# Kernel optimization log

Hardware: AMD Instinct MI355X
Metric: run time of the kernel (lower is better)

The kernel has to match this reference:

```python
import jax, jax.numpy as jnp
import numpy as np

K = 3          # number of nearest neighbors (init kwarg k)
EPS = 1e-16    # PyG knn_interpolate clamps squared distance at 1e-16


def setup_inputs() -> dict:
    key = jax.random.key(0)
    ks = jax.random.split(key, 8)
    N, M, C_IN, C_SKIP, H = 4096, 16384, 256, 128, 256
    x = jax.random.normal(ks[0], (N, C_IN), dtype=jnp.float32)
    pos = jax.random.normal(ks[1], (N, 3), dtype=jnp.float32)
    x_skip = jax.random.normal(ks[2], (M, C_SKIP), dtype=jnp.float32)
    pos_skip = jax.random.normal(ks[3], (M, 3), dtype=jnp.float32)
    W1 = jax.random.normal(ks[4], (C_IN + C_SKIP, H), dtype=jnp.float32) * (1.0 / np.sqrt(C_IN + C_SKIP))
    b1 = jnp.zeros((H,), dtype=jnp.float32)
    W2 = jax.random.normal(ks[5], (H, H), dtype=jnp.float32) * (1.0 / np.sqrt(H))
    b2 = jnp.zeros((H,), dtype=jnp.float32)
    return {"x": x, "pos": pos, "x_skip": x_skip, "pos_skip": pos_skip,
            "W1": W1, "b1": b1, "W2": W2, "b2": b2}


def knn_interpolate(x, pos, pos_skip):
    # squared pairwise distances [M, N]
    d2 = (jnp.sum(pos_skip * pos_skip, -1, keepdims=True)
          - 2.0 * pos_skip @ pos.T
          + jnp.sum(pos * pos, -1))
    neg_d, idx = jax.lax.top_k(-d2, K)          # k smallest distances
    w = 1.0 / jnp.maximum(-neg_d, EPS)           # [M, K] inverse-distance weights
    feats = x[idx]                               # [M, K, C] gather
    return jnp.einsum('mk,mkc->mc', w, feats) / jnp.sum(w, -1, keepdims=True)


def reference(x, pos, x_skip, pos_skip, W1, b1, W2, b2):
    y = knn_interpolate(x, pos, pos_skip)                # [M, C_in]
    h = jnp.concatenate([y, x_skip], axis=-1)            # [M, C_in + C_skip]
    h = jax.nn.relu(h @ W1 + b1)
    return h @ W2 + b2                                    # [M, H]
```

## Files before the change

### kernel.cpp

```cpp
#include <hip/hip_runtime.h>
#include <hip/hip_bf16.h>

#define N_PTS 4096
#define M_PTS 16384
#define CIN   256
#define CSK   128
#define KDIM  384
#define HDIM  256
#define NSHARD 32
#define SHPTS (N_PTS / NSHARD)

typedef unsigned int  u32;
typedef unsigned short u16;
typedef __attribute__((ext_vector_type(8))) short bf16x8;
typedef __attribute__((ext_vector_type(4))) float f32x4;

__device__ __forceinline__ u16 f2bf(float f) {
    union { float f; u32 i; } w; w.f = f;
    u32 x = w.i;
    u32 r = x + 0x7fffu + ((x >> 16) & 1u);
    return (u16)(r >> 16);
}

__device__ __forceinline__ bool ltk(float s, int p, float t, int i) {
    return (s < t) || (s == t && p < i);
}
__device__ __forceinline__ void ins3(float s, int p,
                                     float& t0, float& t1, float& t2,
                                     int& i0, int& i1, int& i2) {
    if (ltk(s, p, t2, i2)) {
        if (ltk(s, p, t1, i1)) {
            t2 = t1; i2 = i1;
            if (ltk(s, p, t0, i0)) { t1 = t0; i1 = i0; t0 = s; i0 = p; }
            else                   { t1 = s;  i1 = p; }
        } else { t2 = s; i2 = p; }
    }
}

#define INS3BL(s, p, t0, t1, t2, i0, i1, i2)                              \
    {                                                                     \
        float _o0 = t0, _o1 = t1, _o2 = t2;                               \
        int _a0 = i0, _a1 = i1, _a2 = i2;                                 \
        bool _c0 = (s) < _o0, _c1 = (s) < _o1, _c2 = (s) < _o2;           \
        t0 = _c0 ? (s) : _o0;              i0 = _c0 ? (p) : _a0;          \
        t1 = _c0 ? _o0 : (_c1 ? (s) : _o1); i1 = _c0 ? _a0 : (_c1 ? (p) : _a1); \
        t2 = _c1 ? _o1 : (_c2 ? (s) : _o2); i2 = _c1 ? _a1 : (_c2 ? (p) : _a2); \
    }

#define INS3MM(s, p, t0, t1, t2, i0, i1, i2)                              \
    {                                                                     \
        bool _c0 = (s) < t0, _c1 = (s) < t1, _c2 = (s) < t2;              \
        int _oi0 = i0, _oi1 = i1;                                         \
        i0 = _c0 ? (p) : i0;                                              \
        i1 = _c0 ? _oi0 : (_c1 ? (p) : i1);                               \
        i2 = _c1 ? _oi1 : (_c2 ? (p) : i2);                               \
        float _ot0 = t0, _ot1 = t1;                                       \
        t0 = fminf(t0, (s));                                              \
        t1 = __builtin_amdgcn_fmed3f(_ot0, t1, (s));                      \
        t2 = __builtin_amdgcn_fmed3f(_ot1, t2, (s));                      \
    }

__global__ __launch_bounds__(256, 8) void knn_scanM(
    const float* __restrict__ pos,
    const float* __restrict__ pos_skip,
    float* __restrict__ candM)
{
    __shared__ float4 spts[SHPTS];
    const int tid = threadIdx.x;
    const int sh = blockIdx.y;
    const int pbase = sh * SHPTS;
    const int m0 = blockIdx.x * 512 + tid;
    const int m1 = m0 + 256;

    if (tid < SHPTS) {
        const int i = pbase + tid;
        float px = pos[3 * i], py = pos[3 * i + 1], pz = pos[3 * i + 2];
        float pn = __fadd_rn(__fadd_rn(__fmul_rn(px, px), __fmul_rn(py, py)),
                             __fmul_rn(pz, pz));
        spts[tid] = make_float4(px, py, pz, pn);
    }

    const float qx0 = pos_skip[3 * m0];
    const float qy0 = pos_skip[3 * m0 + 1];
    const float qz0 = pos_skip[3 * m0 + 2];
    const float qn0 = __fadd_rn(__fadd_rn(__fmul_rn(qx0, qx0), __fmul_rn(qy0, qy0)),
                                __fmul_rn(qz0, qz0));
    const float qx1 = pos_skip[3 * m1];
    const float qy1 = pos_skip[3 * m1 + 1];
    const float qz1 = pos_skip[3 * m1 + 2];
    const float qn1 = __fadd_rn(__fadd_rn(__fmul_rn(qx1, qx1), __fmul_rn(qy1, qy1)),
                                __fmul_rn(qz1, qz1));
    __syncthreads();

    float e[2][2];
    e[0][0] = 3.4e38f; e[0][1] = 3.4e38f;
    e[1][0] = 3.4e38f; e[1][1] = 3.4e38f;

    #pragma unroll 8
    for (int j = 0; j < SHPTS; ++j) {
        float4 v = spts[j];
        const int c = j & 1;
        {
            float b = __fmaf_rn(qz0, v.z, __fmaf_rn(qy0, v.y, __fmul_rn(qx0, v.x)));
            float s = __fadd_rn(__fmaf_rn(-2.0f, b, qn0), v.w);
            e[0][c] = fminf(e[0][c], s);
        }
        {
            float b = __fmaf_rn(qz1, v.z, __fmaf_rn(qy1, v.y, __fmul_rn(qx1, v.x)));
            float s = __fadd_rn(__fmaf_rn(-2.0f, b, qn1), v.w);
            e[1][c] = fminf(e[1][c], s);
        }
    }

    candM[(size_t)sh * M_PTS + m0] = fminf(e[0][0], e[0][1]);
    candM[(size_t)sh * M_PTS + m1] = fminf(e[1][0], e[1][1]);
}

__global__ __launch_bounds__(256) void knn_maskS(
    const float* __restrict__ candM,
    u32* __restrict__ shsel)
{
    const int m = blockIdx.x * 256 + threadIdx.x;
    float t0 = 3.4e38f, t1 = 3.4e38f, t2 = 3.4e38f;
    int   s0 = 63, s1 = 63, s2 = 63;
    #pragma unroll
    for (int sh = 0; sh < NSHARD; ++sh) {
        float mn = candM[(size_t)sh * M_PTS + m];
        INS3BL(mn, sh, t0, t1, t2, s0, s1, s2);
    }
    shsel[m] = (u32)s0 | ((u32)s1 << 8) | ((u32)s2 << 16);
}

__global__ __launch_bounds__(256) void knn_rescan_merge(
    const float* __restrict__ pos,
    const float* __restrict__ pos_skip,
    const u32* __restrict__ shsel,
    float4* __restrict__ nbrw, uint4* __restrict__ nbri)
{
    __shared__ float sv[64][3][3];
    __shared__ int   si[64][3][3];
    const int tid  = threadIdx.x;
    const int ql   = tid >> 2;
    const int slot = tid & 3;
    const int m = blockIdx.x * 64 + ql;

    const u32 sel = shsel[m];

    if (slot < 3) {
        const int sh = (sel >> (8 * slot)) & 63;
        const int pb = sh * SHPTS;

        const float qx = pos_skip[3 * m];
        const float qy = pos_skip[3 * m + 1];
        const float qz = pos_skip[3 * m + 2];
        const float qn = __fadd_rn(__fadd_rn(__fmul_rn(qx, qx), __fmul_rn(qy, qy)),
                                   __fmul_rn(qz, qz));

        float t0 = 3.4e38f, t1 = 3.4e38f, t2 = 3.4e38f;
        int   i0 = 0x7fffffff, i1 = 0x7fffffff, i2 = 0x7fffffff;

        #pragma unroll 4
        for (int j = 0; j < SHPTS; ++j) {
            const int p = pb + j;
            float px = pos[3 * p], py = pos[3 * p + 1], pz = pos[3 * p + 2];
            float pn = __fadd_rn(__fadd_rn(__fmul_rn(px, px), __fmul_rn(py, py)),
                                 __fmul_rn(pz, pz));
            float b = __fmaf_rn(qz, pz, __fmaf_rn(qy, py, __fmul_rn(qx, px)));
            float s = __fadd_rn(__fmaf_rn(-2.0f, b, qn), pn);
            INS3MM(s, p, t0, t1, t2, i0, i1, i2);
        }
        sv[ql][slot][0] = t0; sv[ql][slot][1] = t1; sv[ql][slot][2] = t2;
        si[ql][slot][0] = i0; si[ql][slot][1] = i1; si[ql][slot][2] = i2;
    }
    __syncthreads();

    if (slot == 0) {
        float t0 = 3.4e38f, t1 = 3.4e38f, t2 = 3.4e38f;
        int   i0 = 0x7fffffff, i1 = 0x7fffffff, i2 = 0x7fffffff;
        #pragma unroll
        for (int s = 0; s < 3; ++s)
            #pragma unroll
            for (int k = 0; k < 3; ++k)
                ins3(sv[ql][s][k], si[ql][s][k], t0, t1, t2, i0, i1, i2);

        float w0 = __fdiv_rn(1.0f, fmaxf(t0, 1e-16f));
        float w1 = __fdiv_rn(1.0f, fmaxf(t1, 1e-16f));
        float w2 = __fdiv_rn(1.0f, fmaxf(t2, 1e-16f));
        float inv = __fdiv_rn(1.0f, __fadd_rn(__fadd_rn(w0, w1), w2));
        nbrw[m] = make_float4(w0 * inv, w1 * inv, w2 * inv, 0.f);
        nbri[m] = make_uint4((u32)i0, (u32)i1, (u32)i2, 0u);
    }
}

__global__ __launch_bounds__(256) void gemm_Z(
    const float* __restrict__ x, const float* __restrict__ W1,
    float* __restrict__ Z)
{
    __shared__ alignas(16) u16 Bs[64][40];
    const int tid = threadIdx.x;
    const int w = tid >> 6, l = tid & 63;
    const int bm = blockIdx.x * 128;
    const int bn = blockIdx.y * 64;
    const int lr = l & 15, lg = l >> 4;

    f32x4 acc[2][4];
    #pragma unroll
    for (int mt = 0; mt < 2; ++mt)
        #pragma unroll
        for (int nt = 0; nt < 4; ++nt)
            acc[mt][nt] = (f32x4){0.f, 0.f, 0.f, 0.f};

    const int sc = tid >> 2;
    const int sk = (tid & 3) * 8;

    for (int k0 = 0; k0 < CIN; k0 += 32) {
        #pragma unroll
        for (int j = 0; j < 8; ++j)
            Bs[sc][sk + j] = f2bf(W1[(size_t)(k0 + sk + j) * HDIM + bn + sc]);
        __syncthreads();

        bf16x8 af[2];
        #pragma unroll
        for (int mt = 0; mt < 2; ++mt) {
            const float* xp = x + (size_t)(bm + w * 32 + mt * 16 + lr) * CIN + k0 + lg * 8;
            float4 h0 = *reinterpret_cast<const float4*>(xp);
            float4 h1 = *reinterpret_cast<const float4*>(xp + 4);
            af[mt][0] = (short)f2bf(h0.x); af[mt][1] = (short)f2bf(h0.y);
            af[mt][2] = (short)f2bf(h0.z); af[mt][3] = (short)f2bf(h0.w);
            af[mt][4] = (short)f2bf(h1.x); af[mt][5] = (short)f2bf(h1.y);
            af[mt][6] = (short)f2bf(h1.z); af[mt][7] = (short)f2bf(h1.w);
        }
        #pragma unroll
        for (int nt = 0; nt < 4; ++nt) {
            bf16x8 bf = *reinterpret_cast<const bf16x8*>(&Bs[nt * 16 + lr][lg * 8]);
            #pragma unroll
            for (int mt = 0; mt < 2; ++mt)
                acc[mt][nt] = __builtin_amdgcn_mfma_f32_16x16x32_bf16(
                    af[mt], bf, acc[mt][nt], 0, 0, 0);
        }
        __syncthreads();
    }

    #pragma unroll
    for (int nt = 0; nt < 4; ++nt) {
        const int col = bn + nt * 16 + lr;
        #pragma unroll
        for (int mt = 0; mt < 2; ++mt)
            #pragma unroll
            for (int i = 0; i < 4; ++i) {
                const int row = bm + w * 32 + mt * 16 + lg * 4 + i;
                Z[(size_t)row * HDIM + col] = acc[mt][nt][i];
            }
    }
}

__global__ __launch_bounds__(256) void gemm_SH(
    const float* __restrict__ x_skip, const float* __restrict__ W1,
    const float* __restrict__ b1, const float* __restrict__ Z,
    const float4* __restrict__ nbrw, const uint4* __restrict__ nbri,
    u16* __restrict__ H)
{
    __shared__ alignas(16) u16 Bs[64][40];
    const int tid = threadIdx.x;
    const int w = tid >> 6, l = tid & 63;
    const int bm = blockIdx.x * 128;
    const int bn = blockIdx.y * 64;
    const int lr = l & 15, lg = l >> 4;

    f32x4 acc[2][4];
    #pragma unroll
    for (int mt = 0; mt < 2; ++mt)
        #pragma unroll
        for (int nt = 0; nt < 4; ++nt)
            acc[mt][nt] = (f32x4){0.f, 0.f, 0.f, 0.f};

    const int sc = tid >> 2;
    const int sk = (tid & 3) * 8;

    for (int k0 = 0; k0 < CSK; k0 += 32) {
        #pragma unroll
        for (int j = 0; j < 8; ++j)
            Bs[sc][sk + j] = f2bf(W1[(size_t)(CIN + k0 + sk + j) * HDIM + bn + sc]);
        __syncthreads();

        bf16x8 af[2];
        #pragma unroll
        for (int mt = 0; mt < 2; ++mt) {
            const float* xp = x_skip + (size_t)(bm + w * 32 + mt * 16 + lr) * CSK + k0 + lg * 8;
            float4 h0 = *reinterpret_cast<const float4*>(xp);
            float4 h1 = *reinterpret_cast<const float4*>(xp + 4);
            af[mt][0] = (short)f2bf(h0.x); af[mt][1] = (short)f2bf(h0.y);
            af[mt][2] = (short)f2bf(h0.z); af[mt][3] = (short)f2bf(h0.w);
            af[mt][4] = (short)f2bf(h1.x); af[mt][5] = (short)f2bf(h1.y);
            af[mt][6] = (short)f2bf(h1.z); af[mt][7] = (short)f2bf(h1.w);
        }
        #pragma unroll
        for (int nt = 0; nt < 4; ++nt) {
            bf16x8 bf = *reinterpret_cast<const bf16x8*>(&Bs[nt * 16 + lr][lg * 8]);
            #pragma unroll
            for (int mt = 0; mt < 2; ++mt)
                acc[mt][nt] = __builtin_amdgcn_mfma_f32_16x16x32_bf16(
                    af[mt], bf, acc[mt][nt], 0, 0, 0);
        }
        __syncthreads();
    }

    #pragma unroll
    for (int mt = 0; mt < 2; ++mt) {
        #pragma unroll
        for (int i = 0; i < 4; ++i) {
            const int row = bm + w * 32 + mt * 16 + lg * 4 + i;
            const float4 wv = nbrw[row];
            const uint4  iv = nbri[row];
            const float* z0 = Z + (size_t)(iv.x & 4095u) * HDIM;
            const float* z1 = Z + (size_t)(iv.y & 4095u) * HDIM;
            const float* z2 = Z + (size_t)(iv.z & 4095u) * HDIM;
            #pragma unroll
            for (int nt = 0; nt < 4; ++nt) {
                const int col = bn + nt * 16 + lr;
                float zb = wv.x * z0[col] + wv.y * z1[col] + wv.z * z2[col];
                float v = acc[mt][nt][i] + zb + b1[col];
                H[(size_t)row * HDIM + col] = f2bf(v > 0.f ? v : 0.f);
            }
        }
    }
}

__global__ __launch_bounds__(256) void gemm2_mfma(
    const u16* __restrict__ H, const float* __restrict__ W2,
    const float* __restrict__ b2, float* __restrict__ out)
{
    __shared__ alignas(16) u16 Bs[64][40];
    const int tid = threadIdx.x;
    const int w = tid >> 6, l = tid & 63;
    const int bm = blockIdx.x * 128;
    const int bn = blockIdx.y * 64;
    const int lr = l & 15, lg = l >> 4;

    f32x4 acc[2][4];
    #pragma unroll
    for (int mt = 0; mt < 2; ++mt)
        #pragma unroll
        for (int nt = 0; nt < 4; ++nt)
            acc[mt][nt] = (f32x4){0.f, 0.f, 0.f, 0.f};

    const int sc = tid >> 2;
    const int sk = (tid & 3) * 8;

    for (int k0 = 0; k0 < HDIM; k0 += 32) {
        #pragma unroll
        for (int j = 0; j < 8; ++j)
            Bs[sc][sk + j] = f2bf(W2[(size_t)(k0 + sk + j) * HDIM + bn + sc]);
        __syncthreads();

        bf16x8 af[2];
        #pragma unroll
        for (int mt = 0; mt < 2; ++mt) {
            const int row = bm + w * 32 + mt * 16 + lr;
            af[mt] = *reinterpret_cast<const bf16x8*>(H + (size_t)row * HDIM + k0 + lg * 8);
        }
        #pragma unroll
        for (int nt = 0; nt < 4; ++nt) {
            bf16x8 bf = *reinterpret_cast<const bf16x8*>(&Bs[nt * 16 + lr][lg * 8]);
            #pragma unroll
            for (int mt = 0; mt < 2; ++mt)
                acc[mt][nt] = __builtin_amdgcn_mfma_f32_16x16x32_bf16(
                    af[mt], bf, acc[mt][nt], 0, 0, 0);
        }
        __syncthreads();
    }

    #pragma unroll
    for (int nt = 0; nt < 4; ++nt) {
        const int col = bn + nt * 16 + lr;
        const float bias = b2[col];
        #pragma unroll
        for (int mt = 0; mt < 2; ++mt)
            #pragma unroll
            for (int i = 0; i < 4; ++i) {
                const int row = bm + w * 32 + mt * 16 + lg * 4 + i;
                out[(size_t)row * HDIM + col] = acc[mt][nt][i] + bias;
            }
    }
}

extern "C" void kernel_launch(void* const* d_in, const int* in_sizes, int n_in,
                              void* d_out, int out_size, void* d_ws, size_t ws_size,
                              hipStream_t stream) {
    const float* x        = (const float*)d_in[0];
    const float* pos      = (const float*)d_in[1];
    const float* x_skip   = (const float*)d_in[2];
    const float* pos_skip = (const float*)d_in[3];
    const float* W1       = (const float*)d_in[4];
    const float* b1       = (const float*)d_in[5];
    const float* W2       = (const float*)d_in[6];
    const float* b2       = (const float*)d_in[7];

    u16*    Hbuf = (u16*)d_ws;
    float*  Z    = (float*)((char*)d_ws + (8u << 20));
    float4* nbrw = (float4*)((char*)d_ws + (12u << 20));
    uint4*  nbri = (uint4*)((char*)d_ws + (12u << 20) + (256u << 10));

    float* candM = (float*)d_out;
    u32*   shsel = (u32*)((char*)d_out + (3u << 20));
    float* out   = (float*)d_out;

    knn_scanM       <<<dim3(32, NSHARD), 256, 0, stream>>>(pos, pos_skip, candM);
    knn_maskS       <<<64, 256, 0, stream>>>(candM, shsel);
    knn_rescan_merge<<<256, 256, 0, stream>>>(pos, pos_skip, shsel, nbrw, nbri);
    gemm_Z          <<<dim3(32, 4), 256, 0, stream>>>(x, W1, Z);
    gemm_SH         <<<dim3(128, 4), 256, 0, stream>>>(x_skip, W1, b1, Z, nbrw, nbri, Hbuf);
    gemm2_mfma      <<<dim3(128, 4), 256, 0, stream>>>(Hbuf, W2, b2, out);
}
```

Measured before the change: 70.36 us.

## Merge kNN shard scan with Z GEMM and fold shard selection into rescan

Runs the kNN shard-minimum scan and the independent x@W1 GEMM in one launch, splitting work by block index so the two stages overlap on the GPU. Each scan thread now handles four queries instead of two, which doubles reuse of the shared-memory points and halves the number of scan blocks. The separate shard-mask kernel is removed: its top-3 shard selection is done in parallel by four lanes at the start of the rescan kernel. This cuts the launch count from six to four. The cost is a heterogeneous kernel whose shared memory and register budget are set by the larger branch, which may lower occupancy.

New measurement: 64.07 us. -8.9%, faster.

```diff
diff --git a/kernel.cpp b/kernel.cpp
--- a/kernel.cpp
+++ b/kernel.cpp
@@ -60,91 +60,158 @@
         t2 = __builtin_amdgcn_fmed3f(_ot1, t2, (s));                      \
     }
 
-__global__ __launch_bounds__(256, 8) void knn_scanM(
+__global__ __launch_bounds__(256) void scanM_gemmZ(
     const float* __restrict__ pos,
     const float* __restrict__ pos_skip,
-    float* __restrict__ candM)
+    float* __restrict__ candM,
+    const float* __restrict__ x,
+    const float* __restrict__ W1,
+    float* __restrict__ Z)
 {
-    __shared__ float4 spts[SHPTS];
+    const int bid = blockIdx.x;
     const int tid = threadIdx.x;
-    const int sh = blockIdx.y;
-    const int pbase = sh * SHPTS;
-    const int m0 = blockIdx.x * 512 + tid;
-    const int m1 = m0 + 256;
-
-    if (tid < SHPTS) {
-        const int i = pbase + tid;
-        float px = pos[3 * i], py = pos[3 * i + 1], pz = pos[3 * i + 2];
-        float pn = __fadd_rn(__fadd_rn(__fmul_rn(px, px), __fmul_rn(py, py)),
-                             __fmul_rn(pz, pz));
-        spts[tid] = make_float4(px, py, pz, pn);
-    }
-
-    const float qx0 = pos_skip[3 * m0];
-    const float qy0 = pos_skip[3 * m0 + 1];
-    const float qz0 = pos_skip[3 * m0 + 2];
-    const float qn0 = __fadd_rn(__fadd_rn(__fmul_rn(qx0, qx0), __fmul_rn(qy0, qy0)),
-                                __fmul_rn(qz0, qz0));
-    const float qx1 = pos_skip[3 * m1];
-    const float qy1 = pos_skip[3 * m1 + 1];
-    const float qz1 = pos_skip[3 * m1 + 2];
-    const float qn1 = __fadd_rn(__fadd_rn(__fmul_rn(qx1, qx1), __fmul_rn(qy1, qy1)),
-                                __fmul_rn(qz1, qz1));
-    __syncthreads();
-
-    float e[2][2];
-    e[0][0] = 3.4e38f; e[0][1] = 3.4e38f;
-    e[1][0] = 3.4e38f; e[1][1] = 3.4e38f;
-
-    #pragma unroll 8
-    for (int j = 0; j < SHPTS; ++j) {
-        float4 v = spts[j];
-        const int c = j & 1;
-        {
-            float b = __fmaf_rn(qz0, v.z, __fmaf_rn(qy0, v.y, __fmul_rn(qx0, v.x)));
-            float s = __fadd_rn(__fmaf_rn(-2.0f, b, qn0), v.w);
-            e[0][c] = fminf(e[0][c], s);
-        }
-        {
-            float b = __fmaf_rn(qz1, v.z, __fmaf_rn(qy1, v.y, __fmul_rn(qx1, v.x)));
-            float s = __fadd_rn(__fmaf_rn(-2.0f, b, qn1), v.w);
-            e[1][c] = fminf(e[1][c], s);
-        }
-    }
-
-    candM[(size_t)sh * M_PTS + m0] = fminf(e[0][0], e[0][1]);
-    candM[(size_t)sh * M_PTS + m1] = fminf(e[1][0], e[1][1]);
-}
-
-__global__ __launch_bounds__(256) void knn_maskS(
-    const float* __restrict__ candM,
-    u32* __restrict__ shsel)
-{
-    const int m = blockIdx.x * 256 + threadIdx.x;
-    float t0 = 3.4e38f, t1 = 3.4e38f, t2 = 3.4e38f;
-    int   s0 = 63, s1 = 63, s2 = 63;
-    #pragma unroll
-    for (int sh = 0; sh < NSHARD; ++sh) {
-        float mn = candM[(size_t)sh * M_PTS + m];
-        INS3BL(mn, sh, t0, t1, t2, s0, s1, s2);
-    }
-    shsel[m] = (u32)s0 | ((u32)s1 << 8) | ((u32)s2 << 16);
-}
-
-__global__ __launch_bounds__(256) void knn_rescan_merge(
+
+    if (bid < 512) {
+        __shared__ float4 spts[SHPTS];
+        const int bx = bid & 15, sh = bid >> 4;
+        const int pbase = sh * SHPTS;
+
+        if (tid < SHPTS) {
+            const int i = pbase + tid;
+            float px = pos[3 * i], py = pos[3 * i + 1], pz = pos[3 * i + 2];
+            float pn = __fadd_rn(__fadd_rn(__fmul_rn(px, px), __fmul_rn(py, py)),
+                                 __fmul_rn(pz, pz));
+            spts[tid] = make_float4(px, py, pz, pn);
+        }
+
+        const int mb = bx * 1024 + tid;
+        float qx[4], qy[4], qz[4], qn[4];
+        #pragma unroll
+        for (int q = 0; q < 4; ++q) {
+            const int m = mb + q * 256;
+            qx[q] = pos_skip[3 * m];
+            qy[q] = pos_skip[3 * m + 1];
+            qz[q] = pos_skip[3 * m + 2];
+            qn[q] = __fadd_rn(__fadd_rn(__fmul_rn(qx[q], qx[q]), __fmul_rn(qy[q], qy[q])),
+                              __fmul_rn(qz[q], qz[q]));
+        }
+        __syncthreads();
+
+        float e[4] = {3.4e38f, 3.4e38f, 3.4e38f, 3.4e38f};
+
+        #pragma unroll 8
+        for (int j = 0; j < SHPTS; ++j) {
+            float4 v = spts[j];
+            #pragma unroll
+            for (int q = 0; q < 4; ++q) {
+                float b = __fmaf_rn(qz[q], v.z, __fmaf_rn(qy[q], v.y, __fmul_rn(qx[q], v.x)));
+                float s = __fadd_rn(__fmaf_rn(-2.0f, b, qn[q]), v.w);
+                e[q] = fminf(e[q], s);
+            }
+        }
+
+        #pragma unroll
+        for (int q = 0; q < 4; ++q)
+            candM[(size_t)sh * M_PTS + mb + q * 256] = e[q];
+    } else {
+        __shared__ alignas(16) u16 Bs[64][40];
+        const int id = bid - 512;
+        const int w = tid >> 6, l = tid & 63;
+        const int bm = (id & 31) * 128;
+        const int bn = (id >> 5) * 64;
+        const int lr = l & 15, lg = l >> 4;
+
+        f32x4 acc[2][4];
+        #pragma unroll
+        for (int mt = 0; mt < 2; ++mt)
+            #pragma unroll
+            for (int nt = 0; nt < 4; ++nt)
+                acc[mt][nt] = (f32x4){0.f, 0.f, 0.f, 0.f};
+
+        const int sc = tid >> 2;
+        const int sk = (tid & 3) * 8;
+
+        for (int k0 = 0; k0 < CIN; k0 += 32) {
+            #pragma unroll
+            for (int j = 0; j < 8; ++j)
+                Bs[sc][sk + j] = f2bf(W1[(size_t)(k0 + sk + j) * HDIM + bn + sc]);
+            __syncthreads();
+
+            bf16x8 af[2];
+            #pragma unroll
+            for (int mt = 0; mt < 2; ++mt) {
+                const float* xp = x + (size_t)(bm + w * 32 + mt * 16 + lr) * CIN + k0 + lg * 8;
+                float4 h0 = *reinterpret_cast<const float4*>(xp);
+                float4 h1 = *reinterpret_cast<const float4*>(xp + 4);
+                af[mt][0] = (short)f2bf(h0.x); af[mt][1] = (short)f2bf(h0.y);
+                af[mt][2] = (short)f2bf(h0.z); af[mt][3] = (short)f2bf(h0.w);
+                af[mt][4] = (short)f2bf(h1.x); af[mt][5] = (short)f2bf(h1.y);
+                af[mt][6] = (short)f2bf(h1.z); af[mt][7] = (short)f2bf(h1.w);
+            }
+            #pragma unroll
+            for (int nt = 0; nt < 4; ++nt) {
+                bf16x8 bf = *reinterpret_cast<const bf16x8*>(&Bs[nt * 16 + lr][lg * 8]);
+                #pragma unroll
+                for (int mt = 0; mt < 2; ++mt)
+                    acc[mt][nt] = __builtin_amdgcn_mfma_f32_16x16x32_bf16(
+                        af[mt], bf, acc[mt][nt], 0, 0, 0);
+            }
+            __syncthreads();
+        }
+
+        #pragma unroll
+        for (int nt = 0; nt < 4; ++nt) {
+            const int col = bn + nt * 16 + lr;
+            #pragma unroll
+            for (int mt = 0; mt < 2; ++mt)
+                #pragma unroll
+                for (int i = 0; i < 4; ++i) {
+                    const int row = bm + w * 32 + mt * 16 + lg * 4 + i;
+                    Z[(size_t)row * HDIM + col] = acc[mt][nt][i];
+                }
+        }
+    }
+}
+
+__global__ __launch_bounds__(256) void knn_select_rescan(
     const float* __restrict__ pos,
     const float* __restrict__ pos_skip,
-    const u32* __restrict__ shsel,
+    const float* __restrict__ candM,
     float4* __restrict__ nbrw, uint4* __restrict__ nbri)
 {
-    __shared__ float sv[64][3][3];
-    __shared__ int   si[64][3][3];
+    __shared__ float sv[64][4][3];
+    __shared__ int   si[64][4][3];
+    __shared__ u32   ssel[64];
     const int tid  = threadIdx.x;
     const int ql   = tid >> 2;
     const int slot = tid & 3;
     const int m = blockIdx.x * 64 + ql;
 
-    const u32 sel = shsel[m];
+    {
+        float t0 = 3.4e38f, t1 = 3.4e38f, t2 = 3.4e38f;
+        int   s0 = 63, s1 = 63, s2 = 63;
+        #pragma unroll
+        for (int k = 0; k < 8; ++k) {
+            const int sh = slot * 8 + k;
+            float mn = candM[(size_t)sh * M_PTS + m];
+            INS3BL(mn, sh, t0, t1, t2, s0, s1, s2);
+        }
+        sv[ql][slot][0] = t0; sv[ql][slot][1] = t1; sv[ql][slot][2] = t2;
+        si[ql][slot][0] = s0; si[ql][slot][1] = s1; si[ql][slot][2] = s2;
+    }
+    __syncthreads();
+    if (slot == 0) {
+        float t0 = 3.4e38f, t1 = 3.4e38f, t2 = 3.4e38f;
+        int   s0 = 63, s1 = 63, s2 = 63;
+        #pragma unroll
+        for (int s = 0; s < 4; ++s)
+            #pragma unroll
+            for (int k = 0; k < 3; ++k)
+                ins3(sv[ql][s][k], si[ql][s][k], t0, t1, t2, s0, s1, s2);
+        ssel[ql] = (u32)s0 | ((u32)s1 << 8) | ((u32)s2 << 16);
+    }
+    __syncthreads();
+    const u32 sel = ssel[ql];
 
     if (slot < 3) {
         const int sh = (sel >> (8 * slot)) & 63;
@@ -189,68 +256,6 @@
         float inv = __fdiv_rn(1.0f, __fadd_rn(__fadd_rn(w0, w1), w2));
         nbrw[m] = make_float4(w0 * inv, w1 * inv, w2 * inv, 0.f);
         nbri[m] = make_uint4((u32)i0, (u32)i1, (u32)i2, 0u);
-    }
-}
-
-__global__ __launch_bounds__(256) void gemm_Z(
-    const float* __restrict__ x, const float* __restrict__ W1,
-    float* __restrict__ Z)
-{
-    __shared__ alignas(16) u16 Bs[64][40];
-    const int tid = threadIdx.x;
-    const int w = tid >> 6, l = tid & 63;
-    const int bm = blockIdx.x * 128;
-    const int bn = blockIdx.y * 64;
-    const int lr = l & 15, lg = l >> 4;
-
-    f32x4 acc[2][4];
-    #pragma unroll
-    for (int mt = 0; mt < 2; ++mt)
-        #pragma unroll
-        for (int nt = 0; nt < 4; ++nt)
-            acc[mt][nt] = (f32x4){0.f, 0.f, 0.f, 0.f};
-
-    const int sc = tid >> 2;
-    const int sk = (tid & 3) * 8;
-
-    for (int k0 = 0; k0 < CIN; k0 += 32) {
-        #pragma unroll
-        for (int j = 0; j < 8; ++j)
-            Bs[sc][sk + j] = f2bf(W1[(size_t)(k0 + sk + j) * HDIM + bn + sc]);
-        __syncthreads();
-
-        bf16x8 af[2];
-        #pragma unroll
-        for (int mt = 0; mt < 2; ++mt) {
-            const float* xp = x + (size_t)(bm + w * 32 + mt * 16 + lr) * CIN + k0 + lg * 8;
-            float4 h0 = *reinterpret_cast<const float4*>(xp);
-            float4 h1 = *reinterpret_cast<const float4*>(xp + 4);
-            af[mt][0] = (short)f2bf(h0.x); af[mt][1] = (short)f2bf(h0.y);
-            af[mt][2] = (short)f2bf(h0.z); af[mt][3] = (short)f2bf(h0.w);
-            af[mt][4] = (short)f2bf(h1.x); af[mt][5] = (short)f2bf(h1.y);
-            af[mt][6] = (short)f2bf(h1.z); af[mt][7] = (short)f2bf(h1.w);
-        }
-        #pragma unroll
-        for (int nt = 0; nt < 4; ++nt) {
-            bf16x8 bf = *reinterpret_cast<const bf16x8*>(&Bs[nt * 16 + lr][lg * 8]);
-            #pragma unroll
-            for (int mt = 0; mt < 2; ++mt)
-                acc[mt][nt] = __builtin_amdgcn_mfma_f32_16x16x32_bf16(
-                    af[mt], bf, acc[mt][nt], 0, 0, 0);
-        }
-        __syncthreads();
-    }
-
-    #pragma unroll
-    for (int nt = 0; nt < 4; ++nt) {
-        const int col = bn + nt * 16 + lr;
-        #pragma unroll
-        for (int mt = 0; mt < 2; ++mt)
-            #pragma unroll
-            for (int i = 0; i < 4; ++i) {
-                const int row = bm + w * 32 + mt * 16 + lg * 4 + i;
-                Z[(size_t)row * HDIM + col] = acc[mt][nt][i];
-            }
     }
 }
 
@@ -402,13 +407,10 @@
     uint4*  nbri = (uint4*)((char*)d_ws + (12u << 20) + (256u << 10));
 
     float* candM = (float*)d_out;
-    u32*   shsel = (u32*)((char*)d_out + (3u << 20));
     float* out   = (float*)d_out;
 
-    knn_scanM       <<<dim3(32, NSHARD), 256, 0, stream>>>(pos, pos_skip, candM);
-    knn_maskS       <<<64, 256, 0, stream>>>(candM, shsel);
-    knn_rescan_merge<<<256, 256, 0, stream>>>(pos, pos_skip, shsel, nbrw, nbri);
-    gemm_Z          <<<dim3(32, 4), 256, 0, stream>>>(x, W1, Z);
-    gemm_SH         <<<dim3(128, 4), 256, 0, stream>>>(x_skip, W1, b1, Z, nbrw, nbri, Hbuf);
-    gemm2_mfma      <<<dim3(128, 4), 256, 0, stream>>>(Hbuf, W2, b2, out);
-}
+    scanM_gemmZ      <<<640, 256, 0, stream>>>(pos, pos_skip, candM, x, W1, Z);
+    knn_select_rescan<<<256, 256, 0, stream>>>(pos, pos_skip, candM, nbrw, nbri);
+    gemm_SH          <<<dim3(128, 4), 256, 0, stream>>>(x_skip, W1, b1, Z, nbrw, nbri, Hbuf);
+    gemm2_mfma       <<<dim3(128, 4), 256, 0, stream>>>(Hbuf, W2, b2, out);
+}
```
